# Kernel tuning notes

Measured on AMD Instinct MI355X. Metric: run time of the kernel, lower is better.

Reference implementation:

```python
import jax, jax.numpy as jnp
import numpy as np

B, T, C = 2, 2048, 2048
N_HEAD = 16
N_KV_HEAD = 16
HEAD_DIM = C // N_HEAD  # 128
KV_LORA = C // 2        # 1024
KV_PE = KV_LORA // 4    # 256
KV_CONTENT = KV_LORA - KV_PE  # 768
EPS = 1.1920929e-07  # torch.finfo(float32).eps, F.rms_norm default


def _rms_norm(x):
    # unlearned RMSNorm over last dim
    return x * jax.lax.rsqrt(jnp.mean(x * x, axis=-1, keepdims=True) + EPS)


def _apply_rotary(x, cos, sin):
    # x: (B,T,H,D); cos,sin: (1,T,1,D/2)
    d = x.shape[-1] // 2
    x1, x2 = x[..., :d], x[..., d:]
    return jnp.concatenate([x1 * cos + x2 * sin, -x1 * sin + x2 * cos], axis=-1)


def setup_inputs() -> dict:
    key = jax.random.key(0)
    ks = jax.random.split(key, 9)
    x = jax.random.normal(ks[0], (B, T, C), dtype=jnp.float32)
    # realistic RoPE tables (values bounded like real cos/sin)
    half = HEAD_DIM // 2
    inv_freq = 1.0 / (10000.0 ** (np.arange(0, half, dtype=np.float32) / half))
    tpos = np.arange(T, dtype=np.float32)
    ang = np.einsum('t,d->td', tpos, inv_freq)
    cos = jnp.asarray(np.cos(ang))[None, :, None, :]
    sin = jnp.asarray(np.sin(ang))[None, :, None, :]
    s = 0.02
    wq_a = jax.random.normal(ks[1], (C, KV_LORA), dtype=jnp.float32) * s
    wq_b = jax.random.normal(ks[2], (KV_LORA, N_HEAD * HEAD_DIM), dtype=jnp.float32) * s
    wkv_a = jax.random.normal(ks[3], (C, KV_LORA), dtype=jnp.float32) * s
    wk_b = jax.random.normal(ks[4], (KV_CONTENT, N_KV_HEAD * HEAD_DIM), dtype=jnp.float32) * s
    wkpe_b = jax.random.normal(ks[5], (KV_PE, N_KV_HEAD * HEAD_DIM), dtype=jnp.float32) * s
    wv_b = jax.random.normal(ks[6], (KV_CONTENT, N_KV_HEAD * HEAD_DIM), dtype=jnp.float32) * s
    wo = jax.random.normal(ks[7], (C, C), dtype=jnp.float32) * s
    return dict(x=x, cos=cos, sin=sin, wq_a=wq_a, wq_b=wq_b, wkv_a=wkv_a,
                wk_b=wk_b, wkpe_b=wkpe_b, wv_b=wv_b, wo=wo)


def reference(x, cos, sin, wq_a, wq_b, wkv_a, wk_b, wkpe_b, wv_b, wo):
    Bx, Tx, Cx = x.shape
    # low-rank Q path
    q = (x @ wq_a) @ wq_b                      # (B,T,H*D)
    q = q.reshape(Bx, Tx, N_HEAD, HEAD_DIM)
    # low-rank KV path with pe/content split
    kv_latent = x @ wkv_a                       # (B,T,KV_LORA)
    kv_pe = kv_latent[..., :KV_PE]
    kv_content = kv_latent[..., KV_PE:]
    k_content = (kv_content @ wk_b).reshape(Bx, Tx, N_KV_HEAD, HEAD_DIM)
    k_pe = (kv_pe @ wkpe_b).reshape(Bx, Tx, N_KV_HEAD, HEAD_DIM)
    k = k_content + _apply_rotary(k_pe, cos, sin)
    v = (kv_content @ wv_b).reshape(Bx, Tx, N_KV_HEAD, HEAD_DIM)
    # QK RMSNorm (unlearned)
    q = _rms_norm(q)
    k = _rms_norm(k)
    # SDPA, causal (kv_cache=None path); n_head == n_kv_head
    qh = q.transpose(0, 2, 1, 3)  # (B,H,T,D)
    kh = k.transpose(0, 2, 1, 3)
    vh = v.transpose(0, 2, 1, 3)
    scale = 1.0 / jnp.sqrt(jnp.asarray(HEAD_DIM, dtype=x.dtype))
    scores = jnp.einsum('bhqd,bhkd->bhqk', qh, kh) * scale
    causal = jnp.tril(jnp.ones((Tx, Tx), dtype=bool))
    scores = jnp.where(causal[None, None], scores, jnp.asarray(-jnp.inf, dtype=scores.dtype))
    probs = jax.nn.softmax(scores, axis=-1)
    y = jnp.einsum('bhqk,bhkd->bhqd', probs, vh)
    y = y.transpose(0, 2, 1, 3).reshape(Bx, Tx, Cx)
    return y @ wo
```

## Files before the change

### kernel.cpp

```cpp
#include <hip/hip_runtime.h>
#include <cstddef>
#include <cstdint>

#define TT 2048
#define HH 16
#define EPSV 1.1920929e-07f
#define QSCALE 0.08838834764831845f
#define LOG2E 1.4426950408889634f
#define THRL 11.0f

typedef short bfv8 __attribute__((ext_vector_type(8)));
typedef short bfv4 __attribute__((ext_vector_type(4)));
typedef float f32x4 __attribute__((ext_vector_type(4)));
typedef unsigned u32x2 __attribute__((ext_vector_type(2)));

__device__ __forceinline__ short f2bf(float f) {
    unsigned u = __builtin_bit_cast(unsigned, f);
    u += 0x7FFFu + ((u >> 16) & 1u);
    return (short)(u >> 16);
}
__device__ __forceinline__ float bf2f(short s) {
    unsigned u = ((unsigned)(unsigned short)s) << 16;
    return __builtin_bit_cast(float, u);
}
__device__ __forceinline__ bfv8 pack8(const float4 a, const float4 b) {
    bfv8 r;
    r[0]=f2bf(a.x); r[1]=f2bf(a.y); r[2]=f2bf(a.z); r[3]=f2bf(a.w);
    r[4]=f2bf(b.x); r[5]=f2bf(b.y); r[6]=f2bf(b.z); r[7]=f2bf(b.w);
    return r;
}
__device__ __forceinline__ void gload16(const void* g, void* l) {
    __builtin_amdgcn_global_load_lds(
        (const __attribute__((address_space(1))) unsigned int*)g,
        (__attribute__((address_space(3))) unsigned int*)l, 16, 0, 0);
}
__device__ __forceinline__ unsigned cvtpk(float a, float b) {
    unsigned r;
    asm("v_cvt_pk_bf16_f32 %0, %1, %2" : "=v"(r) : "v"(a), "v"(b));
    return r;
}
__device__ __forceinline__ float fexp2(float x) {
    float y;
    asm volatile("v_exp_f32 %0, %1\n\ts_nop 1" : "=v"(y) : "v"(x));
    return y;
}
__device__ __forceinline__ float bperm(float v, int addr) {
    return __builtin_bit_cast(float,
        __builtin_amdgcn_ds_bpermute(addr, __builtin_bit_cast(int, v)));
}
__device__ __forceinline__ bfv4 mkfrag(float a, float b, float c, float d) {
    u32x2 t; t[0] = cvtpk(a, b); t[1] = cvtpk(c, d);
    return __builtin_bit_cast(bfv4, t);
}

__global__ __launch_bounds__(256) void convx(const float* __restrict__ src,
                                             short* __restrict__ dst, int n8)
{
    int i = blockIdx.x * blockDim.x + threadIdx.x;
    int stride = gridDim.x * blockDim.x;
    for (; i < n8; i += stride) {
        float4 a = ((const float4*)src)[2*i], b = ((const float4*)src)[2*i+1];
        ((bfv8*)dst)[i] = pack8(a, b);
    }
}

__global__ __launch_bounds__(256) void wtrans(const float* __restrict__ src,
                                              short* __restrict__ dst, int R, int C)
{
    __shared__ short tile[64][72];
    const int tid = threadIdx.x;
    const int r0 = blockIdx.y * 64, c0 = blockIdx.x * 64;
    {
        const int i = tid >> 2, c = (tid & 3) * 16;
        const float* sp = src + ((size_t)(r0 + i)) * C + c0 + c;
        float4 v0 = ((const float4*)sp)[0], v1 = ((const float4*)sp)[1];
        float4 v2 = ((const float4*)sp)[2], v3 = ((const float4*)sp)[3];
        *(bfv8*)&tile[i][c]     = pack8(v0, v1);
        *(bfv8*)&tile[i][c + 8] = pack8(v2, v3);
    }
    __syncthreads();
    {
        const int j = tid >> 2, rc = (tid & 3) * 16;
        bfv8 g0, g1;
#pragma unroll
        for (int jj = 0; jj < 8; ++jj) { g0[jj] = tile[rc + jj][j]; g1[jj] = tile[rc + 8 + jj][j]; }
        short* dp = dst + ((size_t)(c0 + j)) * R + r0 + rc;
        *(bfv8*)dp       = g0;
        *(bfv8*)(dp + 8) = g1;
    }
}

template<int OUT_MODE>
__global__ __launch_bounds__(256) void gemm_bf16(
    const short* __restrict__ A, int lda,
    const short* __restrict__ B, int ldb,
    void* __restrict__ Cptr, int ldc, int K)
{
    __shared__ short As[2][128 * 32];
    __shared__ short Bs[2][128 * 32];
    const int tid = threadIdx.x;
    const int w = tid >> 6, lane = tid & 63;
    const int lr = lane & 15, lg = lane >> 4;
    const int wr = w >> 1, wc = w & 1;
    const size_t bm = (size_t)blockIdx.y * 128, bn = (size_t)blockIdx.x * 128;

    f32x4 acc[4][4] = {};

    const int r0 = tid >> 2, ch = (tid & 3) * 8;
    const short* aB0 = A + (bm + r0) * (size_t)lda + ch;
    const short* aB1 = aB0 + 64 * (size_t)lda;
    const short* bB0 = B + (bn + r0) * (size_t)ldb + ch;
    const short* bB1 = bB0 + 64 * (size_t)ldb;
    const int wof = w * 512;

    gload16(aB0, As[0] + wof);
    gload16(aB1, As[0] + wof + 2048);
    gload16(bB0, Bs[0] + wof);
    gload16(bB1, Bs[0] + wof + 2048);
    __syncthreads();

    int cur = 0;
    for (int k0 = 0; k0 < K; k0 += 32) {
        if (k0 + 32 < K) {
            gload16(aB0 + k0 + 32, As[cur ^ 1] + wof);
            gload16(aB1 + k0 + 32, As[cur ^ 1] + wof + 2048);
            gload16(bB0 + k0 + 32, Bs[cur ^ 1] + wof);
            gload16(bB1 + k0 + 32, Bs[cur ^ 1] + wof + 2048);
        }
        bfv8 af[4], bfr[4];
#pragma unroll
        for (int i = 0; i < 4; ++i) {
            af[i]  = *(const bfv8*)&As[cur][(wr * 64 + i * 16 + lr) * 32 + lg * 8];
            bfr[i] = *(const bfv8*)&Bs[cur][(wc * 64 + i * 16 + lr) * 32 + lg * 8];
        }
#pragma unroll
        for (int i = 0; i < 4; ++i)
#pragma unroll
            for (int j = 0; j < 4; ++j)
                acc[i][j] = __builtin_amdgcn_mfma_f32_16x16x32_bf16(af[i], bfr[j], acc[i][j], 0, 0, 0);
        __syncthreads();
        cur ^= 1;
    }

    const size_t crow = bm + wr * 64 + 4 * lg;
    const size_t ccol = bn + wc * 64 + lr;
#pragma unroll
    for (int i = 0; i < 4; ++i)
#pragma unroll
        for (int j = 0; j < 4; ++j)
#pragma unroll
            for (int r = 0; r < 4; ++r) {
                size_t off = (crow + i * 16 + r) * (size_t)ldc + ccol + j * 16;
                if (OUT_MODE == 0) ((float*)Cptr)[off] = acc[i][j][r];
                else               ((short*)Cptr)[off] = f2bf(acc[i][j][r]);
            }
}

__global__ __launch_bounds__(256) void finalize_k(
    const short* __restrict__ kc, const short* __restrict__ pe,
    const float* __restrict__ cosb, const float* __restrict__ sinb,
    short* __restrict__ kb)
{
    const int gw = blockIdx.x * 4 + (threadIdx.x >> 6);
    const int l = threadIdx.x & 63;
    const int r = gw >> 4, h = gw & 15;
    const int t = r & (TT - 1), b = r >> 11;
    const size_t kcb = (size_t)r * 4096 + h * 128;
    const size_t peb = (size_t)r * 2048 + h * 128;

    float x1 = bf2f(pe[peb + l]), x2 = bf2f(pe[peb + 64 + l]);
    float c = cosb[t * 64 + l], s = sinb[t * 64 + l];
    float lo = bf2f(kc[kcb + l])      + x1 * c + x2 * s;
    float hi = bf2f(kc[kcb + 64 + l]) - x1 * s + x2 * c;

    float ss = lo * lo + hi * hi;
#pragma unroll
    for (int o = 32; o; o >>= 1) ss += __shfl_xor(ss, o);
    float rr = rsqrtf(ss * (1.0f / 128.0f) + EPSV);
    const size_t ob = (((size_t)b * HH + h) * TT + t) * 128;
    kb[ob + l]      = f2bf(lo * rr);
    kb[ob + 64 + l] = f2bf(hi * rr);
}

__global__ __launch_bounds__(256) void vtrans(
    const short* __restrict__ src, short* __restrict__ dst)
{
    __shared__ short tile[64][72];
    const int tt = blockIdx.x, dt = blockIdx.y, bh = blockIdx.z;
    const int tid = threadIdx.x;
    {
        const int i = tid >> 2, c = (tid & 3) * 16;
        const size_t sb = ((size_t)((bh >> 4) * TT + tt * 64 + i)) * 4096 + 2048 + (bh & 15) * 128 + dt * 64 + c;
        *(bfv8*)&tile[i][c]     = *(const bfv8*)&src[sb];
        *(bfv8*)&tile[i][c + 8] = *(const bfv8*)&src[sb + 8];
    }
    __syncthreads();
    {
        const int j = tid >> 2, rc = (tid & 3) * 16;
        bfv8 g0, g1;
#pragma unroll
        for (int jj = 0; jj < 8; ++jj) { g0[jj] = tile[rc + jj][j]; g1[jj] = tile[rc + 8 + jj][j]; }
        const size_t db = (((size_t)bh) * 128 + dt * 64 + j) * TT + tt * 64 + rc;
        *(bfv8*)&dst[db]     = g0;
        *(bfv8*)&dst[db + 8] = g1;
    }
}

__device__ __forceinline__ void qk_dual(const short* __restrict__ Ks,
    const bfv8 aq1[4], const bfv8 aq2[4], f32x4 s1[4], f32x4 s2[4], int lr, int lg)
{
    const int swz = lr & 7;
#pragma unroll
    for (int ct = 0; ct < 4; ++ct) {
        f32x4 a1 = {0.f, 0.f, 0.f, 0.f}, a2 = {0.f, 0.f, 0.f, 0.f};
        const int row = ct * 16 + lr;
#pragma unroll
        for (int ks = 0; ks < 4; ++ks) {
            const bfv8 bk = *(const bfv8*)&Ks[row * 128 + (((ks * 4 + lg) ^ swz) * 8)];
            a1 = __builtin_amdgcn_mfma_f32_16x16x32_bf16(bk, aq1[ks], a1, 0, 0, 0);
            a2 = __builtin_amdgcn_mfma_f32_16x16x32_bf16(bk, aq2[ks], a2, 0, 0, 0);
        }
        s1[ct] = a1; s2[ct] = a2;
    }
}

__device__ __forceinline__ void qk_one(const short* __restrict__ Ks,
    const bfv8 aq[4], f32x4 s[4], int lr, int lg)
{
    const int swz = lr & 7;
#pragma unroll
    for (int ct = 0; ct < 4; ++ct) {
        f32x4 a = {0.f, 0.f, 0.f, 0.f};
        const int row = ct * 16 + lr;
#pragma unroll
        for (int ks = 0; ks < 4; ++ks) {
            const bfv8 bk = *(const bfv8*)&Ks[row * 128 + (((ks * 4 + lg) ^ swz) * 8)];
            a = __builtin_amdgcn_mfma_f32_16x16x32_bf16(bk, aq[ks], a, 0, 0, 0);
        }
        s[ct] = a;
    }
}

__device__ __forceinline__ void mask_diag(f32x4 s[4], int lr, int lg, int w)
{
    const int qq = w * 16 + lr;
#pragma unroll
    for (int ct = 0; ct < 4; ++ct)
#pragma unroll
        for (int r = 0; r < 4; ++r)
            if (ct * 16 + 4 * lg + r > qq) s[ct][r] = -__builtin_inff();
}

__device__ __forceinline__ void softmax_lane(f32x4 s[4], float& m, float& l,
                                             f32x4 o[8], int a0)
{
    float c0 = fmaxf(fmaxf(s[0][0], s[0][1]), fmaxf(s[0][2], s[0][3]));
    float c1 = fmaxf(fmaxf(s[1][0], s[1][1]), fmaxf(s[1][2], s[1][3]));
    float c2 = fmaxf(fmaxf(s[2][0], s[2][1]), fmaxf(s[2][2], s[2][3]));
    float c3 = fmaxf(fmaxf(s[3][0], s[3][1]), fmaxf(s[3][2], s[3][3]));
    float mt = fmaxf(fmaxf(c0, c1), fmaxf(c2, c3));
    mt = fmaxf(mt, __shfl_xor(mt, 16));
    mt = fmaxf(mt, __shfl_xor(mt, 32));
    if (!__all(mt - m <= THRL)) {
        float mn = fmaxf(m, mt);
        float alpha = fexp2(m - mn);
        m = mn;
        l *= alpha;
        float av0 = bperm(alpha, a0);
        float av1 = bperm(alpha, a0 + 4);
        float av2 = bperm(alpha, a0 + 8);
        float av3 = bperm(alpha, a0 + 12);
#pragma unroll
        for (int dt = 0; dt < 8; ++dt) {
            o[dt][0] *= av0; o[dt][1] *= av1;
            o[dt][2] *= av2; o[dt][3] *= av3;
        }
    }
    f32x4 acc = {0.f, 0.f, 0.f, 0.f};
#pragma unroll
    for (int ct = 0; ct < 4; ++ct) {
#pragma unroll
        for (int r = 0; r < 4; ++r) s[ct][r] = fexp2(s[ct][r] - m);
        acc += s[ct];
    }
    float rs = (acc[0] + acc[1]) + (acc[2] + acc[3]);
    rs += __shfl_xor(rs, 16);
    rs += __shfl_xor(rs, 32);
    l += rs;
}

__device__ __forceinline__ void p_store(short (&Psw)[16][72], const f32x4 s[4],
                                        int lr, int lg)
{
#pragma unroll
    for (int ct = 0; ct < 4; ++ct)
        *(bfv4*)&Psw[lr][ct * 16 + 4 * lg] = mkfrag(s[ct][0], s[ct][1], s[ct][2], s[ct][3]);
}

__device__ __forceinline__ void pv_dual(const short* __restrict__ Vs,
    const short (&P1)[16][72], const short (&P2)[16][72],
    f32x4 o1[8], f32x4 o2[8], int lr, int lg)
{
    const bfv8 pa0 = *(const bfv8*)&P1[lr][lg * 8];
    const bfv8 pa1 = *(const bfv8*)&P1[lr][32 + lg * 8];
    const bfv8 pb0 = *(const bfv8*)&P2[lr][lg * 8];
    const bfv8 pb1 = *(const bfv8*)&P2[lr][32 + lg * 8];
    const int swz = lr & 7;
#pragma unroll
    for (int dt = 0; dt < 8; ++dt) {
        const int row = dt * 16 + lr;
        const bfv8 bv0 = *(const bfv8*)&Vs[row * 64 + ((lg ^ swz) * 8)];
        const bfv8 bv1 = *(const bfv8*)&Vs[row * 64 + (((4 + lg) ^ swz) * 8)];
        o1[dt] = __builtin_amdgcn_mfma_f32_16x16x32_bf16(pa0, bv0, o1[dt], 0, 0, 0);
        o1[dt] = __builtin_amdgcn_mfma_f32_16x16x32_bf16(pa1, bv1, o1[dt], 0, 0, 0);
        o2[dt] = __builtin_amdgcn_mfma_f32_16x16x32_bf16(pb0, bv0, o2[dt], 0, 0, 0);
        o2[dt] = __builtin_amdgcn_mfma_f32_16x16x32_bf16(pb1, bv1, o2[dt], 0, 0, 0);
    }
}

__device__ __forceinline__ void pv_one(const short* __restrict__ Vs,
    const short (&P2)[16][72], f32x4 o[8], int lr, int lg)
{
    const bfv8 pa0 = *(const bfv8*)&P2[lr][lg * 8];
    const bfv8 pa1 = *(const bfv8*)&P2[lr][32 + lg * 8];
    const int swz = lr & 7;
#pragma unroll
    for (int dt = 0; dt < 8; ++dt) {
        const int row = dt * 16 + lr;
        const bfv8 bv0 = *(const bfv8*)&Vs[row * 64 + ((lg ^ swz) * 8)];
        const bfv8 bv1 = *(const bfv8*)&Vs[row * 64 + (((4 + lg) ^ swz) * 8)];
        o[dt] = __builtin_amdgcn_mfma_f32_16x16x32_bf16(pa0, bv0, o[dt], 0, 0, 0);
        o[dt] = __builtin_amdgcn_mfma_f32_16x16x32_bf16(pa1, bv1, o[dt], 0, 0, 0);
    }
}

__global__ __launch_bounds__(256) void attn_kernel(
    const short* __restrict__ qg, const short* __restrict__ kg,
    const short* __restrict__ vg, short* __restrict__ y)
{
    __shared__ short Ks[64 * 128];
    __shared__ short Vs[128 * 64];
    __shared__ short Ps1[4][16][72];
    __shared__ short Ps2[4][16][72];

    const int lin = blockIdx.x + 16 * blockIdx.y + 256 * blockIdx.z;
    const int work = (lin & 7) * 64 + (lin >> 3);
    const int pi = work & 15, h = (work >> 4) & 15, b = work >> 8;
    const int qt1 = pi, qt2 = 31 - pi;
    const int tid = threadIdx.x, w = tid >> 6, lane = tid & 63;
    const int lr = lane & 15, lg = lane >> 4;
    const int a0 = lg * 80;

    const size_t tok0 = ((size_t)b * HH + h) * TT;

    bfv8 aq1[4], aq2[4];
    {
        const size_t q1 = ((size_t)b * TT + qt1 * 64 + w * 16 + lr) * 2048 + h * 128;
        const size_t q2 = ((size_t)b * TT + qt2 * 64 + w * 16 + lr) * 2048 + h * 128;
#pragma unroll
        for (int ks = 0; ks < 4; ++ks) {
            aq1[ks] = *(const bfv8*)&qg[q1 + ks * 32 + lg * 8];
            aq2[ks] = *(const bfv8*)&qg[q2 + ks * 32 + lg * 8];
        }
#pragma unroll
        for (int st = 0; st < 2; ++st) {
            bfv8* aq = st ? aq2 : aq1;
            float ss = 0.f;
#pragma unroll
            for (int ks = 0; ks < 4; ++ks)
#pragma unroll
                for (int j = 0; j < 8; ++j) { float f = bf2f(aq[ks][j]); ss = fmaf(f, f, ss); }
            ss += __shfl_xor(ss, 16);
            ss += __shfl_xor(ss, 32);
            float rr = rsqrtf(ss * (1.0f / 128.0f) + EPSV) * (QSCALE * LOG2E);
#pragma unroll
            for (int ks = 0; ks < 4; ++ks)
#pragma unroll
                for (int j = 0; j < 4; ++j) {
                    unsigned u = cvtpk(bf2f(aq[ks][2 * j]) * rr, bf2f(aq[ks][2 * j + 1]) * rr);
                    aq[ks][2 * j]     = (short)u;
                    aq[ks][2 * j + 1] = (short)(u >> 16);
                }
        }
    }

    f32x4 o1[8] = {}; f32x4 o2[8] = {};
    float m1 = -__builtin_inff(), m2 = -__builtin_inff();
    float l1 = 0.f, l2 = 0.f;

    const size_t vhead = ((size_t)b * HH + h) * (size_t)128 * TT;
    const int krow = tid >> 4, kub = (tid & 15) ^ (krow & 7);
    const int vrow = tid >> 3, vub = (tid & 7) ^ (vrow & 7);
    const int wof = w * 512;

    for (int kt = 0; kt <= qt2; ++kt) {
        {
            const size_t kbase = (tok0 + kt * 64) * 128;
#pragma unroll
            for (int p = 0; p < 4; ++p) {
                gload16(kg + kbase + (p * 16 + krow) * 128 + kub * 8, Ks + wof + p * 2048);
                gload16(vg + vhead + (size_t)(p * 32 + vrow) * TT + kt * 64 + vub * 8,
                        Vs + wof + p * 2048);
            }
        }
        __syncthreads();

        if (kt <= qt1) {
            f32x4 s1[4], s2[4];
            qk_dual(Ks, aq1, aq2, s1, s2, lr, lg);
            if (kt == qt1) mask_diag(s1, lr, lg, w);
            softmax_lane(s1, m1, l1, o1, a0);
            softmax_lane(s2, m2, l2, o2, a0);
            p_store(Ps1[w], s1, lr, lg);
            p_store(Ps2[w], s2, lr, lg);
            pv_dual(Vs, Ps1[w], Ps2[w], o1, o2, lr, lg);
        } else {
            f32x4 s2[4];
            qk_one(Ks, aq2, s2, lr, lg);
            if (kt == qt2) mask_diag(s2, lr, lg, w);
            softmax_lane(s2, m2, l2, o2, a0);
            p_store(Ps2[w], s2, lr, lg);
            pv_one(Vs, Ps2[w], o2, lr, lg);
        }
        __syncthreads();
    }

    float n1 = 1.0f / l1, n2 = 1.0f / l2;
    float iv1[4], iv2[4];
#pragma unroll
    for (int r = 0; r < 4; ++r) {
        iv1[r] = bperm(n1, a0 + 4 * r);
        iv2[r] = bperm(n2, a0 + 4 * r);
    }
#pragma unroll
    for (int r = 0; r < 4; ++r) {
        const size_t y1 = ((size_t)b * TT + qt1 * 64 + w * 16 + 4 * lg + r) * 2048 + h * 128 + lr;
        const size_t y2 = ((size_t)b * TT + qt2 * 64 + w * 16 + 4 * lg + r) * 2048 + h * 128 + lr;
#pragma unroll
        for (int dt = 0; dt < 8; ++dt) {
            y[y1 + dt * 16] = f2bf(o1[dt][r] * iv1[r]);
            y[y2 + dt * 16] = f2bf(o2[dt][r] * iv2[r]);
        }
    }
}

extern "C" void kernel_launch(void* const* d_in, const int* in_sizes, int n_in,
                              void* d_out, int out_size, void* d_ws, size_t ws_size,
                              hipStream_t stream)
{
    const float* x      = (const float*)d_in[0];
    const float* cosb   = (const float*)d_in[1];
    const float* sinb   = (const float*)d_in[2];
    const float* wq_a   = (const float*)d_in[3];
    const float* wq_b   = (const float*)d_in[4];
    const float* wkv_a  = (const float*)d_in[5];
    const float* wk_b   = (const float*)d_in[6];
    const float* wkpe_b = (const float*)d_in[7];
    const float* wv_b   = (const float*)d_in[8];
    const float* wo     = (const float*)d_in[9];

    short* wsp = (short*)d_ws;
    short* W1  = wsp;
    short* W2  = wsp + 4194304;
    short* W3  = wsp + 7340032;
    short* W4  = wsp + 7864320;
    short* W5  = wsp + 9961472;
    short* C1  = wsp + 14155776;
    short* KV2 = wsp + 22544384;
    short* KPE = wsp + 39321600;
    short* KB  = wsp + 47710208;
    short* VB  = wsp + 56098816;
    short* XB  = (short*)d_out;

    dim3 blk(256);

    convx<<<2048, blk, 0, stream>>>(x, XB, 1048576);
    wtrans<<<dim3(16, 32), blk, 0, stream>>>(wq_a,   W1,                2048, 1024);
    wtrans<<<dim3(16, 32), blk, 0, stream>>>(wkv_a,  W1 + 1024 * 2048,  2048, 1024);
    wtrans<<<dim3(32, 12), blk, 0, stream>>>(wk_b,   W2,                 768, 2048);
    wtrans<<<dim3(32, 12), blk, 0, stream>>>(wv_b,   W2 + 2048 * 768,    768, 2048);
    wtrans<<<dim3(32,  4), blk, 0, stream>>>(wkpe_b, W3,                 256, 2048);
    wtrans<<<dim3(32, 16), blk, 0, stream>>>(wq_b,   W4,                1024, 2048);
    wtrans<<<dim3(32, 32), blk, 0, stream>>>(wo,     W5,                2048, 2048);

    gemm_bf16<1><<<dim3(16, 32), blk, 0, stream>>>(XB, 2048, W1, 2048, C1, 2048, 2048);
    gemm_bf16<1><<<dim3(32, 32), blk, 0, stream>>>(C1 + 1280, 2048, W2, 768, KV2, 4096, 768);
    gemm_bf16<1><<<dim3(16, 32), blk, 0, stream>>>(C1 + 1024, 2048, W3, 256, KPE, 2048, 256);

    finalize_k<<<16384, blk, 0, stream>>>(KV2, KPE, cosb, sinb, KB);
    vtrans<<<dim3(32, 2, 32), blk, 0, stream>>>(KV2, VB);

    gemm_bf16<1><<<dim3(16, 32), blk, 0, stream>>>(C1, 2048, W4, 1024, KPE, 2048, 1024);

    attn_kernel<<<dim3(16, 16, 2), blk, 0, stream>>>(KPE, KB, VB, C1);

    gemm_bf16<0><<<dim3(16, 32), blk, 0, stream>>>(C1, 2048, W5, 2048, d_out, 2048, 2048);
}
```

Before: 334.9 us.

## Replace bf16 GEMM with 256x128 tile, 8-wave, swizzled-LDS, XCD-remapped kernel

Replaces the 128x128, 4-wave GEMM with a 512-thread kernel that computes 256x128 tiles over K-steps of 64. Shared memory is XOR-swizzled to avoid bank conflicts, and loads are prefetched two stages ahead using explicit vmcnt waits and raw barriers. Workgroup IDs are remapped across the 8 XCDs so that neighbouring tiles share L2, and MFMA priority is raised around the compute block. It targets better data reuse and latency hiding in all five projection GEMMs, at the cost of more LDS per block (96 KB), fewer blocks, and fragile hand-written wait counts.

Result: slower. 348.2 us (+4.0%).

```diff
diff --git a/kernel.cpp b/kernel.cpp
--- a/kernel.cpp
+++ b/kernel.cpp
@@ -91,69 +91,89 @@
 }
 
 template<int OUT_MODE>
-__global__ __launch_bounds__(256) void gemm_bf16(
+__global__ __launch_bounds__(512) void gemm8(
     const short* __restrict__ A, int lda,
     const short* __restrict__ B, int ldb,
     void* __restrict__ Cptr, int ldc, int K)
 {
-    __shared__ short As[2][128 * 32];
-    __shared__ short Bs[2][128 * 32];
+    __shared__ short Asm[2][256 * 64];
+    __shared__ short Bsm[2][128 * 64];
+
+    const int nwg = gridDim.x * gridDim.y;
+    int lin = blockIdx.y * gridDim.x + blockIdx.x;
+    lin = (lin & 7) * (nwg >> 3) + (lin >> 3);
+    const int bx = lin % gridDim.x, by = lin / gridDim.x;
+
     const int tid = threadIdx.x;
     const int w = tid >> 6, lane = tid & 63;
     const int lr = lane & 15, lg = lane >> 4;
     const int wr = w >> 1, wc = w & 1;
-    const size_t bm = (size_t)blockIdx.y * 128, bn = (size_t)blockIdx.x * 128;
+    const size_t bm = (size_t)by * 256, bn = (size_t)bx * 128;
+
+    const int crow = tid >> 3, cunit = tid & 7;
+    const short* Ag = A + (bm + crow) * (size_t)lda + (cunit ^ (crow & 7)) * 8;
+    const short* Bg = B + (bn + crow) * (size_t)ldb + (cunit ^ (crow & 7)) * 8;
+    const int ldsOff = crow * 64 + cunit * 8;
+
+    auto stage = [&](int kk, int bb) {
+        gload16(Bg + kk,                        &Bsm[bb][ldsOff]);
+        gload16(Bg + (size_t)64 * ldb + kk,     &Bsm[bb][4096 + ldsOff]);
+        gload16(Ag + kk,                        &Asm[bb][ldsOff]);
+        gload16(Ag + (size_t)64 * lda + kk,     &Asm[bb][4096 + ldsOff]);
+        gload16(Ag + (size_t)128 * lda + kk,    &Asm[bb][8192 + ldsOff]);
+        gload16(Ag + (size_t)192 * lda + kk,    &Asm[bb][12288 + ldsOff]);
+    };
 
     f32x4 acc[4][4] = {};
 
-    const int r0 = tid >> 2, ch = (tid & 3) * 8;
-    const short* aB0 = A + (bm + r0) * (size_t)lda + ch;
-    const short* aB1 = aB0 + 64 * (size_t)lda;
-    const short* bB0 = B + (bn + r0) * (size_t)ldb + ch;
-    const short* bB1 = bB0 + 64 * (size_t)ldb;
-    const int wof = w * 512;
-
-    gload16(aB0, As[0] + wof);
-    gload16(aB1, As[0] + wof + 2048);
-    gload16(bB0, Bs[0] + wof);
-    gload16(bB1, Bs[0] + wof + 2048);
-    __syncthreads();
-
-    int cur = 0;
-    for (int k0 = 0; k0 < K; k0 += 32) {
-        if (k0 + 32 < K) {
-            gload16(aB0 + k0 + 32, As[cur ^ 1] + wof);
-            gload16(aB1 + k0 + 32, As[cur ^ 1] + wof + 2048);
-            gload16(bB0 + k0 + 32, Bs[cur ^ 1] + wof);
-            gload16(bB1 + k0 + 32, Bs[cur ^ 1] + wof + 2048);
-        }
-        bfv8 af[4], bfr[4];
-#pragma unroll
-        for (int i = 0; i < 4; ++i) {
-            af[i]  = *(const bfv8*)&As[cur][(wr * 64 + i * 16 + lr) * 32 + lg * 8];
-            bfr[i] = *(const bfv8*)&Bs[cur][(wc * 64 + i * 16 + lr) * 32 + lg * 8];
-        }
-#pragma unroll
-        for (int i = 0; i < 4; ++i)
-#pragma unroll
-            for (int j = 0; j < 4; ++j)
-                acc[i][j] = __builtin_amdgcn_mfma_f32_16x16x32_bf16(af[i], bfr[j], acc[i][j], 0, 0, 0);
-        __syncthreads();
-        cur ^= 1;
-    }
-
-    const size_t crow = bm + wr * 64 + 4 * lg;
-    const size_t ccol = bn + wc * 64 + lr;
-#pragma unroll
-    for (int i = 0; i < 4; ++i)
+    const int NT = K >> 6;
+    stage(0, 0);
+    if (NT > 1) stage(64, 1);
+
+    for (int t = 0; t < NT; ++t) {
+        const int c = t & 1;
+        if (t + 1 < NT) asm volatile("s_waitcnt vmcnt(6)" ::: "memory");
+        else            asm volatile("s_waitcnt vmcnt(0)" ::: "memory");
+        __builtin_amdgcn_s_barrier();
+
+#pragma unroll
+        for (int ksub = 0; ksub < 2; ++ksub) {
+            bfv8 ah[4], bk[4];
+#pragma unroll
+            for (int j = 0; j < 4; ++j) {
+                const int row = wc * 64 + j * 16 + lr;
+                bk[j] = *(const bfv8*)&Bsm[c][row * 64 + (((ksub * 4 + lg) ^ (row & 7)) * 8)];
+            }
+#pragma unroll
+            for (int i = 0; i < 4; ++i) {
+                const int row = wr * 64 + i * 16 + lr;
+                ah[i] = *(const bfv8*)&Asm[c][row * 64 + (((ksub * 4 + lg) ^ (row & 7)) * 8)];
+            }
+            __builtin_amdgcn_s_setprio(1);
+#pragma unroll
+            for (int i = 0; i < 4; ++i)
+#pragma unroll
+                for (int j = 0; j < 4; ++j)
+                    acc[i][j] = __builtin_amdgcn_mfma_f32_16x16x32_bf16(ah[i], bk[j], acc[i][j], 0, 0, 0);
+            __builtin_amdgcn_s_setprio(0);
+        }
+        __builtin_amdgcn_s_barrier();
+        if (t + 2 < NT) stage((t + 2) << 6, c);
+    }
+
+#pragma unroll
+    for (int i = 0; i < 4; ++i) {
+        const size_t r0 = bm + wr * 64 + i * 16 + 4 * lg;
+        const size_t c0 = bn + wc * 64 + lr;
 #pragma unroll
         for (int j = 0; j < 4; ++j)
 #pragma unroll
             for (int r = 0; r < 4; ++r) {
-                size_t off = (crow + i * 16 + r) * (size_t)ldc + ccol + j * 16;
+                const size_t off = (r0 + r) * (size_t)ldc + c0 + j * 16;
                 if (OUT_MODE == 0) ((float*)Cptr)[off] = acc[i][j][r];
                 else               ((short*)Cptr)[off] = f2bf(acc[i][j][r]);
             }
+    }
 }
 
 __global__ __launch_bounds__(256) void finalize_k(
@@ -473,6 +493,7 @@
     short* XB  = (short*)d_out;
 
     dim3 blk(256);
+    dim3 blk8(512);
 
     convx<<<2048, blk, 0, stream>>>(x, XB, 1048576);
     wtrans<<<dim3(16, 32), blk, 0, stream>>>(wq_a,   W1,                2048, 1024);
@@ -483,16 +504,16 @@
     wtrans<<<dim3(32, 16), blk, 0, stream>>>(wq_b,   W4,                1024, 2048);
     wtrans<<<dim3(32, 32), blk, 0, stream>>>(wo,     W5,                2048, 2048);
 
-    gemm_bf16<1><<<dim3(16, 32), blk, 0, stream>>>(XB, 2048, W1, 2048, C1, 2048, 2048);
-    gemm_bf16<1><<<dim3(32, 32), blk, 0, stream>>>(C1 + 1280, 2048, W2, 768, KV2, 4096, 768);
-    gemm_bf16<1><<<dim3(16, 32), blk, 0, stream>>>(C1 + 1024, 2048, W3, 256, KPE, 2048, 256);
+    gemm8<1><<<dim3(16, 16), blk8, 0, stream>>>(XB, 2048, W1, 2048, C1, 2048, 2048);
+    gemm8<1><<<dim3(32, 16), blk8, 0, stream>>>(C1 + 1280, 2048, W2, 768, KV2, 4096, 768);
+    gemm8<1><<<dim3(16, 16), blk8, 0, stream>>>(C1 + 1024, 2048, W3, 256, KPE, 2048, 256);
 
     finalize_k<<<16384, blk, 0, stream>>>(KV2, KPE, cosb, sinb, KB);
     vtrans<<<dim3(32, 2, 32), blk, 0, stream>>>(KV2, VB);
 
-    gemm_bf16<1><<<dim3(16, 32), blk, 0, stream>>>(C1, 2048, W4, 1024, KPE, 2048, 1024);
+    gemm8<1><<<dim3(16, 16), blk8, 0, stream>>>(C1, 2048, W4, 1024, KPE, 2048, 1024);
 
     attn_kernel<<<dim3(16, 16, 2), blk, 0, stream>>>(KPE, KB, VB, C1);
 
-    gemm_bf16<0><<<dim3(16, 32), blk, 0, stream>>>(C1, 2048, W5, 2048, d_out, 2048, 2048);
-}
+    gemm8<0><<<dim3(16, 16), blk8, 0, stream>>>(C1, 2048, W5, 2048, d_out, 2048, 2048);
+}
```

## Merge preprocessing kernels into one launch and write V transposed from GEMM epilogue

Applied to the files above, without the earlier changes.

Replaces the x conversion and seven weight-transpose launches with a single pre_all kernel that dispatches on block index. The K-content/V GEMM is split into two launches, and the V GEMM gets a new epilogue that writes directly into the head-major transposed layout. This removes the separate vtrans kernel and its round trip through memory. The new epilogue writes 4-element bf16 fragments along T with strided addresses, which may coalesce less well than row stores.

Result: faster. 316.2 us (median of 2 runs) (-5.6%).

```diff
diff --git a/kernel.cpp b/kernel.cpp
--- a/kernel.cpp
+++ b/kernel.cpp
@@ -53,26 +53,33 @@
     return __builtin_bit_cast(bfv4, t);
 }
 
-__global__ __launch_bounds__(256) void convx(const float* __restrict__ src,
-                                             short* __restrict__ dst, int n8)
-{
-    int i = blockIdx.x * blockDim.x + threadIdx.x;
-    int stride = gridDim.x * blockDim.x;
-    for (; i < n8; i += stride) {
-        float4 a = ((const float4*)src)[2*i], b = ((const float4*)src)[2*i+1];
-        ((bfv8*)dst)[i] = pack8(a, b);
-    }
-}
-
-__global__ __launch_bounds__(256) void wtrans(const float* __restrict__ src,
-                                              short* __restrict__ dst, int R, int C)
+struct TransDesc { const float* src; short* dst; int R, C, b0; };
+struct TransArgs { TransDesc t[7]; };
+
+__global__ __launch_bounds__(256) void pre_all(TransArgs ta,
+    const float* __restrict__ xsrc, short* __restrict__ xdst, int nx)
 {
     __shared__ short tile[64][72];
+    int bid = blockIdx.x;
+    if (bid < nx) {
+        const int i = bid * 256 + threadIdx.x;
+        float4 a = ((const float4*)xsrc)[2 * i], b = ((const float4*)xsrc)[2 * i + 1];
+        ((bfv8*)xdst)[i] = pack8(a, b);
+        return;
+    }
+    bid -= nx;
+    int e = 0;
+#pragma unroll
+    for (int k = 1; k < 7; ++k) if (bid >= ta.t[k].b0) e = k;
+    const TransDesc D = ta.t[e];
+    const int loc = bid - D.b0;
+    const int cb = D.C >> 6;
+    const int by = loc / cb, bx = loc - by * cb;
     const int tid = threadIdx.x;
-    const int r0 = blockIdx.y * 64, c0 = blockIdx.x * 64;
+    const int r0 = by * 64, c0 = bx * 64;
     {
         const int i = tid >> 2, c = (tid & 3) * 16;
-        const float* sp = src + ((size_t)(r0 + i)) * C + c0 + c;
+        const float* sp = D.src + ((size_t)(r0 + i)) * D.C + c0 + c;
         float4 v0 = ((const float4*)sp)[0], v1 = ((const float4*)sp)[1];
         float4 v2 = ((const float4*)sp)[2], v3 = ((const float4*)sp)[3];
         *(bfv8*)&tile[i][c]     = pack8(v0, v1);
@@ -84,7 +91,7 @@
         bfv8 g0, g1;
 #pragma unroll
         for (int jj = 0; jj < 8; ++jj) { g0[jj] = tile[rc + jj][j]; g1[jj] = tile[rc + 8 + jj][j]; }
-        short* dp = dst + ((size_t)(c0 + j)) * R + r0 + rc;
+        short* dp = D.dst + ((size_t)(c0 + j)) * D.R + r0 + rc;
         *(bfv8*)dp       = g0;
         *(bfv8*)(dp + 8) = g1;
     }
@@ -142,18 +149,34 @@
         cur ^= 1;
     }
 
-    const size_t crow = bm + wr * 64 + 4 * lg;
-    const size_t ccol = bn + wc * 64 + lr;
-#pragma unroll
-    for (int i = 0; i < 4; ++i)
-#pragma unroll
-        for (int j = 0; j < 4; ++j)
-#pragma unroll
-            for (int r = 0; r < 4; ++r) {
-                size_t off = (crow + i * 16 + r) * (size_t)ldc + ccol + j * 16;
-                if (OUT_MODE == 0) ((float*)Cptr)[off] = acc[i][j][r];
-                else               ((short*)Cptr)[off] = f2bf(acc[i][j][r]);
+    if (OUT_MODE == 2) {
+        short* out = (short*)Cptr;
+        const size_t bb = bm >> 11;
+        const int tb = (int)(bm & 2047) + wr * 64 + 4 * lg;
+        const int colb = (int)bn + wc * 64 + lr;
+#pragma unroll
+        for (int i = 0; i < 4; ++i)
+#pragma unroll
+            for (int j = 0; j < 4; ++j) {
+                const int c = colb + j * 16;
+                const int h = c >> 7, d = c & 127;
+                const size_t idx = (((bb * HH + h) * 128 + d) << 11) + tb + i * 16;
+                *(bfv4*)&out[idx] = mkfrag(acc[i][j][0], acc[i][j][1], acc[i][j][2], acc[i][j][3]);
             }
+    } else {
+        const size_t crow = bm + wr * 64 + 4 * lg;
+        const size_t ccol = bn + wc * 64 + lr;
+#pragma unroll
+        for (int i = 0; i < 4; ++i)
+#pragma unroll
+            for (int j = 0; j < 4; ++j)
+#pragma unroll
+                for (int r = 0; r < 4; ++r) {
+                    size_t off = (crow + i * 16 + r) * (size_t)ldc + ccol + j * 16;
+                    if (OUT_MODE == 0) ((float*)Cptr)[off] = acc[i][j][r];
+                    else               ((short*)Cptr)[off] = f2bf(acc[i][j][r]);
+                }
+    }
 }
 
 __global__ __launch_bounds__(256) void finalize_k(
@@ -165,7 +188,7 @@
     const int l = threadIdx.x & 63;
     const int r = gw >> 4, h = gw & 15;
     const int t = r & (TT - 1), b = r >> 11;
-    const size_t kcb = (size_t)r * 4096 + h * 128;
+    const size_t kcb = (size_t)r * 2048 + h * 128;
     const size_t peb = (size_t)r * 2048 + h * 128;
 
     float x1 = bf2f(pe[peb + l]), x2 = bf2f(pe[peb + 64 + l]);
@@ -180,30 +203,6 @@
     const size_t ob = (((size_t)b * HH + h) * TT + t) * 128;
     kb[ob + l]      = f2bf(lo * rr);
     kb[ob + 64 + l] = f2bf(hi * rr);
-}
-
-__global__ __launch_bounds__(256) void vtrans(
-    const short* __restrict__ src, short* __restrict__ dst)
-{
-    __shared__ short tile[64][72];
-    const int tt = blockIdx.x, dt = blockIdx.y, bh = blockIdx.z;
-    const int tid = threadIdx.x;
-    {
-        const int i = tid >> 2, c = (tid & 3) * 16;
-        const size_t sb = ((size_t)((bh >> 4) * TT + tt * 64 + i)) * 4096 + 2048 + (bh & 15) * 128 + dt * 64 + c;
-        *(bfv8*)&tile[i][c]     = *(const bfv8*)&src[sb];
-        *(bfv8*)&tile[i][c + 8] = *(const bfv8*)&src[sb + 8];
-    }
-    __syncthreads();
-    {
-        const int j = tid >> 2, rc = (tid & 3) * 16;
-        bfv8 g0, g1;
-#pragma unroll
-        for (int jj = 0; jj < 8; ++jj) { g0[jj] = tile[rc + jj][j]; g1[jj] = tile[rc + 8 + jj][j]; }
-        const size_t db = (((size_t)bh) * 128 + dt * 64 + j) * TT + tt * 64 + rc;
-        *(bfv8*)&dst[db]     = g0;
-        *(bfv8*)&dst[db + 8] = g1;
-    }
 }
 
 __device__ __forceinline__ void qk_dual(const short* __restrict__ Ks,
@@ -466,29 +465,30 @@
     short* W4  = wsp + 7864320;
     short* W5  = wsp + 9961472;
     short* C1  = wsp + 14155776;
-    short* KV2 = wsp + 22544384;
-    short* KPE = wsp + 39321600;
-    short* KB  = wsp + 47710208;
-    short* VB  = wsp + 56098816;
+    short* KC  = wsp + 22544384;
+    short* KPE = wsp + 30932992;
+    short* KB  = wsp + 39321600;
+    short* VB  = wsp + 47710208;
     short* XB  = (short*)d_out;
 
     dim3 blk(256);
 
-    convx<<<2048, blk, 0, stream>>>(x, XB, 1048576);
-    wtrans<<<dim3(16, 32), blk, 0, stream>>>(wq_a,   W1,                2048, 1024);
-    wtrans<<<dim3(16, 32), blk, 0, stream>>>(wkv_a,  W1 + 1024 * 2048,  2048, 1024);
-    wtrans<<<dim3(32, 12), blk, 0, stream>>>(wk_b,   W2,                 768, 2048);
-    wtrans<<<dim3(32, 12), blk, 0, stream>>>(wv_b,   W2 + 2048 * 768,    768, 2048);
-    wtrans<<<dim3(32,  4), blk, 0, stream>>>(wkpe_b, W3,                 256, 2048);
-    wtrans<<<dim3(32, 16), blk, 0, stream>>>(wq_b,   W4,                1024, 2048);
-    wtrans<<<dim3(32, 32), blk, 0, stream>>>(wo,     W5,                2048, 2048);
+    TransArgs ta;
+    ta.t[0] = {wq_a,   W1,                2048, 1024,    0};
+    ta.t[1] = {wkv_a,  W1 + 1024 * 2048,  2048, 1024,  512};
+    ta.t[2] = {wk_b,   W2,                 768, 2048, 1024};
+    ta.t[3] = {wv_b,   W2 + 2048 * 768,    768, 2048, 1408};
+    ta.t[4] = {wkpe_b, W3,                 256, 2048, 1792};
+    ta.t[5] = {wq_b,   W4,                1024, 2048, 1920};
+    ta.t[6] = {wo,     W5,                2048, 2048, 2432};
+    pre_all<<<4096 + 3456, blk, 0, stream>>>(ta, x, XB, 4096);
 
     gemm_bf16<1><<<dim3(16, 32), blk, 0, stream>>>(XB, 2048, W1, 2048, C1, 2048, 2048);
-    gemm_bf16<1><<<dim3(32, 32), blk, 0, stream>>>(C1 + 1280, 2048, W2, 768, KV2, 4096, 768);
+    gemm_bf16<1><<<dim3(16, 32), blk, 0, stream>>>(C1 + 1280, 2048, W2, 768, KC, 2048, 768);
+    gemm_bf16<2><<<dim3(16, 32), blk, 0, stream>>>(C1 + 1280, 2048, W2 + 2048 * 768, 768, VB, 0, 768);
     gemm_bf16<1><<<dim3(16, 32), blk, 0, stream>>>(C1 + 1024, 2048, W3, 256, KPE, 2048, 256);
 
-    finalize_k<<<16384, blk, 0, stream>>>(KV2, KPE, cosb, sinb, KB);
-    vtrans<<<dim3(32, 2, 32), blk, 0, stream>>>(KV2, VB);
+    finalize_k<<<16384, blk, 0, stream>>>(KC, KPE, cosb, sinb, KB);
 
     gemm_bf16<1><<<dim3(16, 32), blk, 0, stream>>>(C1, 2048, W4, 1024, KPE, 2048, 1024);
 
```
